# Kernel tuning notes

Measured on AMD Instinct MI355X. Metric: run time of the kernel, lower is better.

The kernel has to match this reference:

```python
import jax, jax.numpy as jnp
import numpy as np
import math

NH = 16  # n_head
HS = 64  # head_size = n_embd // n_head


def setup_inputs() -> dict:
    key = jax.random.key(0)
    ks = jax.random.split(key, 7)
    B, T, C, QL, KVL = 2, 2048, 1024, 128, 128
    s = lambda k, shape, fan_in: jax.random.normal(k, shape, jnp.float32) / np.sqrt(fan_in)
    return {
        "x": jax.random.normal(ks[0], (B, T, C), jnp.float32),
        "W_dq": s(ks[1], (QL, C), C),
        "W_uq": s(ks[2], (C, QL), QL),
        "W_dkv": s(ks[3], (KVL, C), C),
        "W_uk": s(ks[4], (C, KVL), KVL),
        "W_uv": s(ks[5], (C, KVL), KVL),
        "W_o": s(ks[6], (C, C), C),
    }


def reference(x, W_dq, W_uq, W_dkv, W_uk, W_uv, W_o):
    B, T, C = x.shape
    kvl = W_dkv.shape[0]
    # absorbed matrices (training branch)
    k_eff = (W_dq.T @ W_uq.T @ W_uk).reshape(NH, HS, kvl)            # (nh, hs, kvl)
    v_eff = (W_uv.T @ W_o.T).reshape(kvl, NH, HS).transpose(1, 0, 2)  # (nh, kvl, hs)
    # latent kv cache
    c_kv = x @ W_dkv.T                                                # (B, T, kvl)
    # query path
    q = (x @ W_dq.T @ W_uq.T).reshape(B, T, NH, HS).transpose(0, 2, 1, 3)  # (B, nh, T, hs)
    # scores: q @ k_eff @ c_kv^T
    ql = jnp.einsum('bhtd,hdl->bhtl', q, k_eff)                       # (B, nh, T, kvl)
    scores = jnp.einsum('bhtl,bsl->bhts', ql, c_kv) / math.sqrt(HS)   # (B, nh, T, T)
    # causal mask
    mask = jnp.tril(jnp.ones((T, T), dtype=bool))
    scores = jnp.where(mask[None, None], scores, -jnp.inf)
    attn = jax.nn.softmax(scores, axis=-1)
    # output: attn @ c_kv @ v_eff
    ctx = jnp.einsum('bhts,bsl->bhtl', attn, c_kv)                    # (B, nh, T, kvl)
    y = jnp.einsum('bhtl,hld->bhtd', ctx, v_eff)                      # (B, nh, T, hs)
    y = y.transpose(0, 2, 1, 3).reshape(B, T, C)
    return y, c_kv
```

## Files before the change

kernel.cpp:

```cpp
#include <hip/hip_runtime.h>
#include <hip/hip_bf16.h>

typedef __hip_bfloat16 bf16;
typedef __attribute__((ext_vector_type(8))) short short8;
typedef __attribute__((ext_vector_type(4))) float f32x4;

#define NHD 16
#define HSD 64
#define KVLD 128
#define QLD 128
#define CD 1024
#define BD 2
#define TD 2048

__device__ __forceinline__ short8 ld8(const bf16* p) { return *(const short8*)p; }
__device__ __forceinline__ void st8(bf16* p, short8 v) { *(short8*)p = v; }

__device__ __forceinline__ void st4(bf16* p, float4 a) {
    union { short4 s; bf16 h[4]; } u;
    u.h[0] = __float2bfloat16(a.x); u.h[1] = __float2bfloat16(a.y);
    u.h[2] = __float2bfloat16(a.z); u.h[3] = __float2bfloat16(a.w);
    *(short4*)p = u.s;
}
__device__ __forceinline__ void st4f(bf16* p, f32x4 a) {
    union { short4 s; bf16 h[4]; } u;
    u.h[0] = __float2bfloat16(a[0]); u.h[1] = __float2bfloat16(a[1]);
    u.h[2] = __float2bfloat16(a[2]); u.h[3] = __float2bfloat16(a[3]);
    *(short4*)p = u.s;
}

__global__ __launch_bounds__(256) void k_pre(const float* __restrict__ wuq,
                                             const float* __restrict__ wuk,
                                             const float* __restrict__ wdq,
                                             const float* __restrict__ wdkv,
                                             float* __restrict__ m1p,
                                             float* __restrict__ G,
                                             bf16* __restrict__ wqkv_bf) {
    const int b = blockIdx.x;
    const int tid = threadIdx.x;
    if (b < 32) {
        const int part = b >> 2, iq = b & 3;
        const int i = iq * 32 + (tid >> 3);
        const int j16 = (tid & 7) << 4;
        float acc[16];
#pragma unroll
        for (int t = 0; t < 16; ++t) acc[t] = 0.f;
        const float* wq = wuq + (size_t)part * 128 * QLD;
        const float* wk = wuk + (size_t)part * 128 * KVLD;
#pragma unroll 2
        for (int c = 0; c < 128; ++c) {
            float a = wq[c * QLD + i];
            const float4* wr = (const float4*)(wk + c * KVLD + j16);
            float4 b0 = wr[0], b1 = wr[1], b2 = wr[2], b3 = wr[3];
            acc[0] += a * b0.x;  acc[1] += a * b0.y;  acc[2] += a * b0.z;  acc[3] += a * b0.w;
            acc[4] += a * b1.x;  acc[5] += a * b1.y;  acc[6] += a * b1.z;  acc[7] += a * b1.w;
            acc[8] += a * b2.x;  acc[9] += a * b2.y;  acc[10] += a * b2.z; acc[11] += a * b2.w;
            acc[12] += a * b3.x; acc[13] += a * b3.y; acc[14] += a * b3.z; acc[15] += a * b3.w;
        }
        float* dst = m1p + (size_t)part * 16384 + (size_t)i * 128 + j16;
#pragma unroll
        for (int q = 0; q < 4; ++q)
            ((float4*)dst)[q] = make_float4(acc[4 * q], acc[4 * q + 1], acc[4 * q + 2], acc[4 * q + 3]);
    } else if (b < 96) {
        const int b1 = b - 32;
        const int h = b1 >> 2, pq = b1 & 3;
        const int p = pq * 32 + (tid >> 3);
        const int i16 = (tid & 7) << 4;
        float acc[16];
#pragma unroll
        for (int t = 0; t < 16; ++t) acc[t] = 0.f;
        const float* wdqp = wdq + (size_t)p * CD + h * 64;
        const float* wuqh = wuq + (size_t)(h * 64) * QLD + i16;
#pragma unroll 2
        for (int d = 0; d < 64; ++d) {
            float a = wdqp[d];
            const float4* wr = (const float4*)(wuqh + d * QLD);
            float4 b0 = wr[0], b1v = wr[1], b2 = wr[2], b3 = wr[3];
            acc[0] += a * b0.x;  acc[1] += a * b0.y;  acc[2] += a * b0.z;  acc[3] += a * b0.w;
            acc[4] += a * b1v.x; acc[5] += a * b1v.y; acc[6] += a * b1v.z; acc[7] += a * b1v.w;
            acc[8] += a * b2.x;  acc[9] += a * b2.y;  acc[10] += a * b2.z; acc[11] += a * b2.w;
            acc[12] += a * b3.x; acc[13] += a * b3.y; acc[14] += a * b3.z; acc[15] += a * b3.w;
        }
        float* dst = G + (size_t)h * 16384 + (size_t)p * 128 + i16;
#pragma unroll
        for (int q = 0; q < 4; ++q)
            ((float4*)dst)[q] = make_float4(acc[4 * q], acc[4 * q + 1], acc[4 * q + 2], acc[4 * q + 3]);
    } else {
        const int r = (b - 96) * 16 + (tid >> 4);
        const int c0 = (tid & 15) << 6;
        const float* src = (r < 128) ? (wdq + (size_t)r * CD) : (wdkv + (size_t)(r - 128) * CD);
#pragma unroll
        for (int t = 0; t < 16; ++t) {
            float4 f = *(const float4*)(src + c0 + t * 4);
            st4(wqkv_bf + (size_t)r * CD + c0 + t * 4, f);
        }
    }
}

__global__ __launch_bounds__(256) void k_main(const float* __restrict__ x,
                                              const bf16* __restrict__ wqkv_bf,
                                              const float* __restrict__ m1p,
                                              const float* __restrict__ G,
                                              const float* __restrict__ wuv,
                                              const float* __restrict__ wo,
                                              bf16* __restrict__ q1_bf,
                                              float* __restrict__ ckv_out,
                                              bf16* __restrict__ ckv_bf,
                                              bf16* __restrict__ ckvT_bf,
                                              bf16* __restrict__ Et_bf,
                                              bf16* __restrict__ veffT_bf) {
    __shared__ __align__(16) short As_raw[16 * 72];
    __shared__ __align__(16) short Bs_raw[256 * 72];
    __shared__ float m1s[1024];
    const int blk = blockIdx.x;
    const int tid = threadIdx.x;

    if (blk < 256) {
        const int m0 = blk * 16;
        const int w = tid >> 6, lane = tid & 63, m16 = lane & 15, g = lane >> 4;
        bf16* As = (bf16*)As_raw;
        bf16* Bs = (bf16*)Bs_raw;

        f32x4 acc[4];
#pragma unroll
        for (int nb = 0; nb < 4; ++nb) acc[nb] = (f32x4){0.f, 0.f, 0.f, 0.f};

        for (int k0 = 0; k0 < CD; k0 += 64) {
            __syncthreads();
            {
                int row = tid >> 4, kc = (tid & 15) << 2;
                float4 f = *(const float4*)(x + (size_t)(m0 + row) * CD + k0 + kc);
                st4(As + row * 72 + kc, f);
            }
#pragma unroll
            for (int kk = 0; kk < 8; ++kk) {
                int v = tid + kk * 256;
                int row = v >> 3, kc = (v & 7) << 3;
                st8(Bs + row * 72 + kc, ld8(wqkv_bf + (size_t)row * CD + k0 + kc));
            }
            __syncthreads();
            short8 aF[2];
#pragma unroll
            for (int kf = 0; kf < 2; ++kf)
                aF[kf] = ld8(As + m16 * 72 + kf * 32 + g * 8);
#pragma unroll
            for (int nb = 0; nb < 4; ++nb)
#pragma unroll
                for (int kf = 0; kf < 2; ++kf) {
                    short8 bF = ld8(Bs + (w * 64 + nb * 16 + m16) * 72 + kf * 32 + g * 8);
                    acc[nb] = __builtin_amdgcn_mfma_f32_16x16x32_bf16(aF[kf], bF, acc[nb], 0, 0, 0);
                }
        }

#pragma unroll
        for (int nb = 0; nb < 4; ++nb)
#pragma unroll
            for (int r = 0; r < 4; ++r) {
                int t = m0 + g * 4 + r;
                int col = w * 64 + nb * 16 + m16;
                float v = acc[nb][r];
                if (col < 128) {
                    q1_bf[(size_t)t * QLD + col] = __float2bfloat16(v);
                } else {
                    int l = col - 128;
                    ckv_out[(size_t)t * KVLD + l] = v;
                    bf16 hv = __float2bfloat16(v);
                    ckv_bf[(size_t)t * KVLD + l] = hv;
                    int b = t >> 11, tl = t & 2047;
                    ckvT_bf[((size_t)b * KVLD + l) * TD + tl] = hv;
                }
            }
    } else if (blk < 512) {
        const int b2 = blk - 256;
        const int h = b2 >> 4, lb = b2 & 15;
        for (int v = tid; v < 1024; v += 256) {
            int p = v >> 3, lq = v & 7;
            float s = 0.f;
#pragma unroll
            for (int part = 0; part < 8; ++part)
                s += m1p[(size_t)part * 16384 + (size_t)p * 128 + lb * 8 + lq];
            m1s[v] = s;
        }
        __syncthreads();
        const int lq = tid >> 5, i4 = (tid & 31) << 2;
        const float* Gh = G + (size_t)h * 16384;
        float4 acc = make_float4(0.f, 0.f, 0.f, 0.f);
#pragma unroll 4
        for (int p = 0; p < 128; ++p) {
            float a = m1s[p * 8 + lq];
            float4 g4 = *(const float4*)(Gh + p * 128 + i4);
            acc.x += a * g4.x; acc.y += a * g4.y;
            acc.z += a * g4.z; acc.w += a * g4.w;
        }
        const float sc = 0.1803368801f;
        const int l = lb * 8 + lq;
        st4(Et_bf + ((size_t)h * 128 + l) * 128 + i4,
            make_float4(sc * acc.x, sc * acc.y, sc * acc.z, sc * acc.w));
    } else {
        const int b3 = blk - 512;
        const int cc = b3 * 4 + (tid >> 6);
        const int l2 = (tid & 63) << 1;
        const float* wor = wo + (size_t)cc * CD;
        float ax = 0.f, ay = 0.f;
#pragma unroll 4
        for (int c0 = 0; c0 < CD; ++c0) {
            float a = wor[c0];
            float2 wv = *(const float2*)(wuv + (size_t)c0 * KVLD + l2);
            ax += a * wv.x; ay += a * wv.y;
        }
        union { short2 s; bf16 h2[2]; } u;
        u.h2[0] = __float2bfloat16(ax);
        u.h2[1] = __float2bfloat16(ay);
        *(short2*)(veffT_bf + (size_t)cc * KVLD + l2) = u.s;
    }
}

__global__ __launch_bounds__(512, 4) void k_flash(const bf16* __restrict__ Q1_bf,
                                                  const bf16* __restrict__ Et_bf,
                                                  const bf16* __restrict__ ckv_bf,
                                                  const bf16* __restrict__ ckvT_bf,
                                                  const bf16* __restrict__ veffT_bf,
                                                  float* __restrict__ yout) {
    const int h = blockIdx.x & 15;
    const int b = blockIdx.x >> 4;
    const int qlo = blockIdx.y;
    const int qhi = 31 - qlo;
    const int tid = threadIdx.x;
    const int w = tid >> 6;
    const int ws = w >> 2;
    const int wq = w & 3;
    const int lane = tid & 63;
    const int m16 = lane & 15;
    const int g = lane >> 4;
    const int myqt = ws ? qlo : qhi;
    const int row0 = myqt * 64;

    __shared__ __align__(16) short smem_raw[28288];
    bf16* smem = (bf16*)smem_raw;
    bf16* kvN = smem;
    bf16* kvT = smem + 8704;
    bf16* pS  = smem + 19072 + w * 1152;
    bf16* bufLo = kvT;
    bf16* vT = smem + 19072;

    {
        const bf16 one = __float2bfloat16(1.0f);
        for (int idx = tid; idx < 16 * 72; idx += 512)
            kvT[9216 + idx] = one;
    }

    {
        const bf16* q1hi = Q1_bf + ((size_t)(b * TD + qhi * 64)) * QLD;
        const bf16* q1lo = Q1_bf + ((size_t)(b * TD + qlo * 64)) * QLD;
#pragma unroll
        for (int k = 0; k < 2; ++k) {
            int v = tid + k * 512;
            int row = v >> 4, cv = (v & 15) << 3;
            st8(kvN + row * 136 + cv, ld8(q1hi + row * QLD + cv));
            st8(bufLo + row * 136 + cv, ld8(q1lo + row * QLD + cv));
        }
    }
    __syncthreads();
    bf16* myQ1 = ws ? bufLo : kvN;
    {
        short8 aq[4];
#pragma unroll
        for (int kf = 0; kf < 4; ++kf)
            aq[kf] = ld8(myQ1 + (wq * 16 + m16) * 136 + kf * 32 + g * 8);
        const bf16* Eh = Et_bf + (size_t)h * QLD * KVLD;
        f32x4 qc[8];
#pragma unroll
        for (int nb = 0; nb < 8; ++nb) qc[nb] = (f32x4){0.f, 0.f, 0.f, 0.f};
#pragma unroll
        for (int nb = 0; nb < 8; ++nb)
#pragma unroll
            for (int kf = 0; kf < 4; ++kf) {
                short8 bq = ld8(Eh + (nb * 16 + m16) * QLD + kf * 32 + g * 8);
                qc[nb] = __builtin_amdgcn_mfma_f32_16x16x32_bf16(aq[kf], bq, qc[nb], 0, 0, 0);
            }
        __syncthreads();
#pragma unroll
        for (int nb = 0; nb < 8; ++nb)
#pragma unroll
            for (int r = 0; r < 4; ++r)
                myQ1[(wq * 16 + g * 4 + r) * 136 + nb * 16 + m16] = __float2bfloat16(qc[nb][r]);
    }
    __syncthreads();
    short8 qlA[4];
#pragma unroll
    for (int kf = 0; kf < 4; ++kf)
        qlA[kf] = ld8(myQ1 + (wq * 16 + m16) * 136 + kf * 32 + g * 8);

    f32x4 cx[9];
#pragma unroll
    for (int nb = 0; nb < 9; ++nb) cx[nb] = (f32x4){0.f, 0.f, 0.f, 0.f};
    float mrow = -INFINITY;
    const int rg = row0 + wq * 16 + m16;

    const bf16* ckb = ckv_bf + (size_t)b * TD * KVLD;
    const bf16* ckTb = ckvT_bf + (size_t)b * KVLD * TD;

    int nrow[2], ncol[2], trow[2], tcol[2];
#pragma unroll
    for (int k = 0; k < 2; ++k) {
        int v = tid + k * 512;
        nrow[k] = v >> 4; ncol[k] = (v & 15) << 3;
        trow[k] = v >> 3; tcol[k] = (v & 7) << 3;
    }
    short8 pfN[2], pfT[2];
#pragma unroll
    for (int k = 0; k < 2; ++k) {
        pfN[k] = ld8(ckb + (size_t)nrow[k] * KVLD + ncol[k]);
        pfT[k] = ld8(ckTb + (size_t)trow[k] * TD + tcol[k]);
    }

    for (int tile = 0; tile <= qhi; ++tile) {
        const int s0 = tile * 64;
        __syncthreads();
#pragma unroll
        for (int k = 0; k < 2; ++k) {
            st8(kvN + nrow[k] * 136 + ncol[k], pfN[k]);
            st8(kvT + trow[k] * 72 + tcol[k], pfT[k]);
        }
        __syncthreads();
        if (tile < qhi) {
            const int s1 = s0 + 64;
#pragma unroll
            for (int k = 0; k < 2; ++k) {
                pfN[k] = ld8(ckb + (size_t)(s1 + nrow[k]) * KVLD + ncol[k]);
                pfT[k] = ld8(ckTb + (size_t)trow[k] * TD + s1 + tcol[k]);
            }
        }

        if (ws == 0 || tile <= qlo) {
            f32x4 sa[4];
#pragma unroll
            for (int nb = 0; nb < 4; ++nb) sa[nb] = (f32x4){0.f, 0.f, 0.f, 0.f};
#pragma unroll
            for (int nb = 0; nb < 4; ++nb)
#pragma unroll
                for (int kf = 0; kf < 4; ++kf) {
                    short8 ak = ld8(kvN + (nb * 16 + m16) * 136 + kf * 32 + g * 8);
                    sa[nb] = __builtin_amdgcn_mfma_f32_16x16x32_bf16(ak, qlA[kf], sa[nb], 0, 0, 0);
                }

            if (tile == myqt) {
#pragma unroll
                for (int nb = 0; nb < 4; ++nb)
#pragma unroll
                    for (int r = 0; r < 4; ++r) {
                        int sg = s0 + nb * 16 + g * 4 + r;
                        if (sg > rg) sa[nb][r] = -INFINITY;
                    }
            }

            float mloc = sa[0][0];
#pragma unroll
            for (int nb = 0; nb < 4; ++nb)
#pragma unroll
                for (int r = 0; r < 4; ++r) mloc = fmaxf(mloc, sa[nb][r]);
            mloc = fmaxf(mloc, __shfl_xor(mloc, 16));
            mloc = fmaxf(mloc, __shfl_xor(mloc, 32));
            if (__any(mloc > mrow)) {
                float mt = fmaxf(mrow, mloc);
                float al = exp2f(mrow - mt);
                mrow = mt;
#pragma unroll
                for (int nb = 0; nb < 9; ++nb)
#pragma unroll
                    for (int r = 0; r < 4; ++r) cx[nb][r] *= al;
            }

#pragma unroll
            for (int nb = 0; nb < 4; ++nb) {
                float4 p4;
                p4.x = exp2f(sa[nb][0] - mrow);
                p4.y = exp2f(sa[nb][1] - mrow);
                p4.z = exp2f(sa[nb][2] - mrow);
                p4.w = exp2f(sa[nb][3] - mrow);
                st4(pS + m16 * 72 + nb * 16 + g * 4, p4);
            }
            __builtin_amdgcn_wave_barrier();

            short8 pA[2];
#pragma unroll
            for (int kf = 0; kf < 2; ++kf)
                pA[kf] = ld8(pS + m16 * 72 + kf * 32 + g * 8);
#pragma unroll
            for (int nb = 0; nb < 9; ++nb)
#pragma unroll
                for (int kf = 0; kf < 2; ++kf) {
                    short8 av = ld8(kvT + (nb * 16 + m16) * 72 + kf * 32 + g * 8);
                    cx[nb] = __builtin_amdgcn_mfma_f32_16x16x32_bf16(av, pA[kf], cx[nb], 0, 0, 0);
                }
        }
    }

    float invl = 1.f / cx[8][0];
#pragma unroll
    for (int nb = 0; nb < 8; ++nb)
#pragma unroll
        for (int r = 0; r < 4; ++r) cx[nb][r] *= invl;
    __syncthreads();
    bf16* ctxS = ws ? bufLo : kvN;
#pragma unroll
    for (int nb = 0; nb < 8; ++nb)
        st4f(ctxS + (wq * 16 + m16) * 136 + nb * 16 + g * 4, cx[nb]);
    {
        const bf16* vsrc = veffT_bf + (size_t)h * HSD * KVLD;
#pragma unroll
        for (int k = 0; k < 2; ++k) {
            int v = tid + k * 512;
            int row = v >> 4, cv = (v & 15) << 3;
            st8(vT + row * 136 + cv, ld8(vsrc + row * KVLD + cv));
        }
    }
    __syncthreads();

    short8 cB[4];
#pragma unroll
    for (int kf = 0; kf < 4; ++kf)
        cB[kf] = ld8(ctxS + (wq * 16 + m16) * 136 + kf * 32 + g * 8);
    f32x4 ya[4];
#pragma unroll
    for (int nb = 0; nb < 4; ++nb) ya[nb] = (f32x4){0.f, 0.f, 0.f, 0.f};
#pragma unroll
    for (int nb = 0; nb < 4; ++nb)
#pragma unroll
        for (int kf = 0; kf < 4; ++kf) {
            short8 av = ld8(vT + (nb * 16 + m16) * 136 + kf * 32 + g * 8);
            ya[nb] = __builtin_amdgcn_mfma_f32_16x16x32_bf16(av, cB[kf], ya[nb], 0, 0, 0);
        }
    float* yo = yout + ((size_t)b * TD + rg) * CD + h * HSD;
#pragma unroll
    for (int nb = 0; nb < 4; ++nb)
        *(float4*)(yo + nb * 16 + g * 4) = *(float4*)&ya[nb];
}

extern "C" void kernel_launch(void* const* d_in, const int* in_sizes, int n_in,
                              void* d_out, int out_size, void* d_ws, size_t ws_size,
                              hipStream_t stream) {
    const float* x    = (const float*)d_in[0];
    const float* wdq  = (const float*)d_in[1];
    const float* wuq  = (const float*)d_in[2];
    const float* wdkv = (const float*)d_in[3];
    const float* wuk  = (const float*)d_in[4];
    const float* wuv  = (const float*)d_in[5];
    const float* wo   = (const float*)d_in[6];
    float* yout = (float*)d_out;
    float* ckv_out = yout + (size_t)BD * TD * CD;

    float* ws = (float*)d_ws;
    float* M1P = ws;
    float* G   = M1P + 131072;
    bf16* wqkv_bf  = (bf16*)(G + 262144);
    bf16* Et_bf    = wqkv_bf + 262144;
    bf16* veffT_bf = Et_bf + 262144;
    bf16* ckv_bf   = veffT_bf + 131072;
    bf16* ckvT_bf  = ckv_bf + 524288;
    bf16* Q1_bf    = ckvT_bf + 524288;

    k_pre <<<112, 256, 0, stream>>>(wuq, wuk, wdq, wdkv, M1P, G, wqkv_bf);
    k_main<<<768, 256, 0, stream>>>(x, wqkv_bf, M1P, G, wuv, wo,
                                    Q1_bf, ckv_out, ckv_bf, ckvT_bf, Et_bf, veffT_bf);

    dim3 grid(32, 16);
    k_flash<<<grid, 512, 0, stream>>>(Q1_bf, Et_bf, ckv_bf, ckvT_bf, veffT_bf, yout);
}
```

Measured before the change: 270.7 us.

## Spread weight-precompute over more blocks and register-prefetch projection GEMM tiles

New measurement: 240.9 us. 11.0% less time.

```diff
diff --git a/kernel.cpp b/kernel.cpp
--- a/kernel.cpp
+++ b/kernel.cpp
@@ -38,61 +38,53 @@
                                              bf16* __restrict__ wqkv_bf) {
     const int b = blockIdx.x;
     const int tid = threadIdx.x;
-    if (b < 32) {
-        const int part = b >> 2, iq = b & 3;
-        const int i = iq * 32 + (tid >> 3);
-        const int j16 = (tid & 7) << 4;
-        float acc[16];
-#pragma unroll
-        for (int t = 0; t < 16; ++t) acc[t] = 0.f;
+    if (b < 128) {
+        const int part = b >> 4, ig = b & 15;
+        const int i = ig * 8 + (tid >> 5);
+        const int j4 = (tid & 31) << 2;
         const float* wq = wuq + (size_t)part * 128 * QLD;
         const float* wk = wuk + (size_t)part * 128 * KVLD;
-#pragma unroll 2
+        float4 acc = make_float4(0.f, 0.f, 0.f, 0.f);
+#pragma unroll 4
         for (int c = 0; c < 128; ++c) {
             float a = wq[c * QLD + i];
-            const float4* wr = (const float4*)(wk + c * KVLD + j16);
-            float4 b0 = wr[0], b1 = wr[1], b2 = wr[2], b3 = wr[3];
-            acc[0] += a * b0.x;  acc[1] += a * b0.y;  acc[2] += a * b0.z;  acc[3] += a * b0.w;
-            acc[4] += a * b1.x;  acc[5] += a * b1.y;  acc[6] += a * b1.z;  acc[7] += a * b1.w;
-            acc[8] += a * b2.x;  acc[9] += a * b2.y;  acc[10] += a * b2.z; acc[11] += a * b2.w;
-            acc[12] += a * b3.x; acc[13] += a * b3.y; acc[14] += a * b3.z; acc[15] += a * b3.w;
-        }
-        float* dst = m1p + (size_t)part * 16384 + (size_t)i * 128 + j16;
-#pragma unroll
-        for (int q = 0; q < 4; ++q)
-            ((float4*)dst)[q] = make_float4(acc[4 * q], acc[4 * q + 1], acc[4 * q + 2], acc[4 * q + 3]);
-    } else if (b < 96) {
-        const int b1 = b - 32;
-        const int h = b1 >> 2, pq = b1 & 3;
-        const int p = pq * 32 + (tid >> 3);
-        const int i16 = (tid & 7) << 4;
-        float acc[16];
-#pragma unroll
-        for (int t = 0; t < 16; ++t) acc[t] = 0.f;
+            float4 kv = *(const float4*)(wk + c * KVLD + j4);
+            acc.x = fmaf(a, kv.x, acc.x); acc.y = fmaf(a, kv.y, acc.y);
+            acc.z = fmaf(a, kv.z, acc.z); acc.w = fmaf(a, kv.w, acc.w);
+        }
+        *(float4*)(m1p + (size_t)part * 16384 + (size_t)i * 128 + j4) = acc;
+    } else if (b < 256) {
+        const int b1 = b - 128;
+        const int h = b1 >> 3, p8 = b1 & 7;
+        const int p = p8 * 16 + (tid >> 4);
+        const int i8 = (tid & 15) << 3;
+        float acc[8];
+#pragma unroll
+        for (int t = 0; t < 8; ++t) acc[t] = 0.f;
         const float* wdqp = wdq + (size_t)p * CD + h * 64;
-        const float* wuqh = wuq + (size_t)(h * 64) * QLD + i16;
+        const float* wuqh = wuq + (size_t)(h * 64) * QLD + i8;
 #pragma unroll 2
         for (int d = 0; d < 64; ++d) {
             float a = wdqp[d];
-            const float4* wr = (const float4*)(wuqh + d * QLD);
-            float4 b0 = wr[0], b1v = wr[1], b2 = wr[2], b3 = wr[3];
-            acc[0] += a * b0.x;  acc[1] += a * b0.y;  acc[2] += a * b0.z;  acc[3] += a * b0.w;
-            acc[4] += a * b1v.x; acc[5] += a * b1v.y; acc[6] += a * b1v.z; acc[7] += a * b1v.w;
-            acc[8] += a * b2.x;  acc[9] += a * b2.y;  acc[10] += a * b2.z; acc[11] += a * b2.w;
-            acc[12] += a * b3.x; acc[13] += a * b3.y; acc[14] += a * b3.z; acc[15] += a * b3.w;
-        }
-        float* dst = G + (size_t)h * 16384 + (size_t)p * 128 + i16;
-#pragma unroll
-        for (int q = 0; q < 4; ++q)
-            ((float4*)dst)[q] = make_float4(acc[4 * q], acc[4 * q + 1], acc[4 * q + 2], acc[4 * q + 3]);
+            float4 b0 = *(const float4*)(wuqh + d * QLD);
+            float4 b1v = *(const float4*)(wuqh + d * QLD + 4);
+            acc[0] = fmaf(a, b0.x, acc[0]);  acc[1] = fmaf(a, b0.y, acc[1]);
+            acc[2] = fmaf(a, b0.z, acc[2]);  acc[3] = fmaf(a, b0.w, acc[3]);
+            acc[4] = fmaf(a, b1v.x, acc[4]); acc[5] = fmaf(a, b1v.y, acc[5]);
+            acc[6] = fmaf(a, b1v.z, acc[6]); acc[7] = fmaf(a, b1v.w, acc[7]);
+        }
+        float* dst = G + (size_t)h * 16384 + (size_t)p * 128 + i8;
+        *(float4*)dst = make_float4(acc[0], acc[1], acc[2], acc[3]);
+        *(float4*)(dst + 4) = make_float4(acc[4], acc[5], acc[6], acc[7]);
     } else {
-        const int r = (b - 96) * 16 + (tid >> 4);
-        const int c0 = (tid & 15) << 6;
+        const int r = (b - 256) * 4 + (tid >> 6);
+        const int lane = tid & 63;
         const float* src = (r < 128) ? (wdq + (size_t)r * CD) : (wdkv + (size_t)(r - 128) * CD);
 #pragma unroll
-        for (int t = 0; t < 16; ++t) {
-            float4 f = *(const float4*)(src + c0 + t * 4);
-            st4(wqkv_bf + (size_t)r * CD + c0 + t * 4, f);
+        for (int k = 0; k < 4; ++k) {
+            int f4 = lane + k * 64;
+            float4 f = ((const float4*)src)[f4];
+            st4(wqkv_bf + (size_t)r * CD + f4 * 4, f);
         }
     }
 }
@@ -121,24 +113,38 @@
         bf16* As = (bf16*)As_raw;
         bf16* Bs = (bf16*)Bs_raw;
 
+        const int arow = tid >> 4, akc = (tid & 15) << 2;
+        const float* axp = x + (size_t)(m0 + arow) * CD + akc;
+        int brow[8], bkc[8];
+#pragma unroll
+        for (int kk = 0; kk < 8; ++kk) {
+            int v = tid + kk * 256;
+            brow[kk] = v >> 3; bkc[kk] = (v & 7) << 3;
+        }
+
+        float4 pA = *(const float4*)(axp);
+        short8 pB[8];
+#pragma unroll
+        for (int kk = 0; kk < 8; ++kk)
+            pB[kk] = ld8(wqkv_bf + (size_t)brow[kk] * CD + bkc[kk]);
+
         f32x4 acc[4];
 #pragma unroll
         for (int nb = 0; nb < 4; ++nb) acc[nb] = (f32x4){0.f, 0.f, 0.f, 0.f};
 
         for (int k0 = 0; k0 < CD; k0 += 64) {
             __syncthreads();
-            {
-                int row = tid >> 4, kc = (tid & 15) << 2;
-                float4 f = *(const float4*)(x + (size_t)(m0 + row) * CD + k0 + kc);
-                st4(As + row * 72 + kc, f);
-            }
-#pragma unroll
-            for (int kk = 0; kk < 8; ++kk) {
-                int v = tid + kk * 256;
-                int row = v >> 3, kc = (v & 7) << 3;
-                st8(Bs + row * 72 + kc, ld8(wqkv_bf + (size_t)row * CD + k0 + kc));
-            }
+            st4(As + arow * 72 + akc, pA);
+#pragma unroll
+            for (int kk = 0; kk < 8; ++kk)
+                st8(Bs + brow[kk] * 72 + bkc[kk], pB[kk]);
             __syncthreads();
+            if (k0 + 64 < CD) {
+                pA = *(const float4*)(axp + k0 + 64);
+#pragma unroll
+                for (int kk = 0; kk < 8; ++kk)
+                    pB[kk] = ld8(wqkv_bf + (size_t)brow[kk] * CD + k0 + 64 + bkc[kk]);
+            }
             short8 aF[2];
 #pragma unroll
             for (int kf = 0; kf < 2; ++kf)
@@ -189,8 +195,8 @@
         for (int p = 0; p < 128; ++p) {
             float a = m1s[p * 8 + lq];
             float4 g4 = *(const float4*)(Gh + p * 128 + i4);
-            acc.x += a * g4.x; acc.y += a * g4.y;
-            acc.z += a * g4.z; acc.w += a * g4.w;
+            acc.x = fmaf(a, g4.x, acc.x); acc.y = fmaf(a, g4.y, acc.y);
+            acc.z = fmaf(a, g4.z, acc.z); acc.w = fmaf(a, g4.w, acc.w);
         }
         const float sc = 0.1803368801f;
         const int l = lb * 8 + lq;
@@ -198,20 +204,27 @@
             make_float4(sc * acc.x, sc * acc.y, sc * acc.z, sc * acc.w));
     } else {
         const int b3 = blk - 512;
-        const int cc = b3 * 4 + (tid >> 6);
-        const int l2 = (tid & 63) << 1;
-        const float* wor = wo + (size_t)cc * CD;
-        float ax = 0.f, ay = 0.f;
+        const int cc0 = b3 * 4;
+        float* woS = (float*)Bs_raw;
+#pragma unroll
+        for (int k = 0; k < 4; ++k) {
+            int f4 = tid + k * 256;
+            ((float4*)woS)[f4] = ((const float4*)(wo + (size_t)cc0 * CD))[f4];
+        }
+        __syncthreads();
+        const int l = tid & 127;
+        const int c2 = (tid >> 7) << 1;
+        const float* w0 = woS + c2 * CD;
+        const float* w1 = woS + (c2 + 1) * CD;
+        float a0 = 0.f, a1 = 0.f;
 #pragma unroll 4
-        for (int c0 = 0; c0 < CD; ++c0) {
-            float a = wor[c0];
-            float2 wv = *(const float2*)(wuv + (size_t)c0 * KVLD + l2);
-            ax += a * wv.x; ay += a * wv.y;
-        }
-        union { short2 s; bf16 h2[2]; } u;
-        u.h2[0] = __float2bfloat16(ax);
-        u.h2[1] = __float2bfloat16(ay);
-        *(short2*)(veffT_bf + (size_t)cc * KVLD + l2) = u.s;
+        for (int c = 0; c < CD; ++c) {
+            float v = wuv[(size_t)c * KVLD + l];
+            a0 = fmaf(w0[c], v, a0);
+            a1 = fmaf(w1[c], v, a1);
+        }
+        veffT_bf[(size_t)(cc0 + c2) * KVLD + l] = __float2bfloat16(a0);
+        veffT_bf[(size_t)(cc0 + c2 + 1) * KVLD + l] = __float2bfloat16(a1);
     }
 }
 
@@ -460,7 +473,7 @@
     bf16* ckvT_bf  = ckv_bf + 524288;
     bf16* Q1_bf    = ckvT_bf + 524288;
 
-    k_pre <<<112, 256, 0, stream>>>(wuq, wuk, wdq, wdkv, M1P, G, wqkv_bf);
+    k_pre <<<320, 256, 0, stream>>>(wuq, wuk, wdq, wdkv, M1P, G, wqkv_bf);
     k_main<<<768, 256, 0, stream>>>(x, wqkv_bf, M1P, G, wuv, wo,
                                     Q1_bf, ckv_out, ckv_bf, ckvT_bf, Et_bf, veffT_bf);
 
```
